# Performance work log

Measured on AMD Instinct MI355X. Metric: run time of the kernel, lower is better.

The kernel has to match this reference:

```python
import jax, jax.numpy as jnp
import numpy as np

N_NODES = 50000
N_EDGES = 800000
IN_DIM = 128
HID_DIM = 128
N_CLS = 64
EPS = 1e-12  # torch F.normalize clamp_min eps


def setup_inputs() -> dict:
    key = jax.random.key(0)
    ks = jax.random.split(key, 10)
    x = jax.random.normal(ks[0], (N_NODES, IN_DIM), dtype=jnp.float32)
    edge_index = jax.random.randint(ks[1], (2, N_EDGES), 0, N_NODES, dtype=jnp.int64)
    C_vals = jax.random.uniform(ks[2], (N_EDGES,), dtype=jnp.float32)
    W1 = jax.random.normal(ks[3], (IN_DIM, HID_DIM), dtype=jnp.float32) * 0.05
    b1 = jax.random.normal(ks[4], (HID_DIM,), dtype=jnp.float32) * 0.05
    W2 = jax.random.normal(ks[5], (HID_DIM, HID_DIM), dtype=jnp.float32) * 0.05
    b2 = jax.random.normal(ks[6], (HID_DIM,), dtype=jnp.float32) * 0.05
    W3 = jax.random.normal(ks[7], (HID_DIM, N_CLS), dtype=jnp.float32) * 0.05
    b3 = jax.random.normal(ks[8], (N_CLS,), dtype=jnp.float32) * 0.05
    return {"x": x, "edge_index": edge_index, "C_vals": C_vals,
            "W1": W1, "b1": b1, "W2": W2, "b2": b2, "W3": W3, "b3": b3}


def _spmm(row, col, vals, h, n):
    # C @ h with C sparse COO: out[row] += vals * h[col]
    return jax.ops.segment_sum(vals[:, None] * h[col], row, num_segments=n)


def reference(x, edge_index, C_vals, W1, b1, W2, b2, W3, b3):
    n = x.shape[0]
    row, col = edge_index[0], edge_index[1]

    def layer(h, W, b, last):
        prop = _spmm(row, col, C_vals, h, n)          # [N, d_in]
        h = prop @ W + b                              # Linear
        if not last:
            h = jax.nn.relu(h)
            # dropout inactive in eval mode; L2 normalize rows (norm=True)
            nrm = jnp.maximum(jnp.linalg.norm(h, axis=1, keepdims=True), EPS)
            h = h / nrm
        return h

    h = layer(x, W1, b1, False)
    h = layer(h, W2, b2, False)
    h = layer(h, W3, b3, True)
    return h
```

## Files before the change

kernel.cpp:

```cpp
#include <hip/hip_runtime.h>
#include <hip/hip_fp16.h>

#define NN 50000
#define NE 800000
#define DIM 128
#define NB ((NN + 255) / 256)

typedef _Float16 half8 __attribute__((ext_vector_type(8)));
typedef float f32x4 __attribute__((ext_vector_type(4)));

__global__ __launch_bounds__(256) void edge_histo_pos(const int* __restrict__ ei,
                                                      int* __restrict__ cnt,
                                                      int* __restrict__ pos) {
  int e = blockIdx.x * 256 + threadIdx.x;
  if (e >= NE) return;
  int r = ei[e], c = ei[NE + e];
  int p = -1;
  if ((unsigned)r < NN && (unsigned)c < NN) p = atomicAdd(&cnt[r], 1);
  pos[e] = p;
}

__global__ __launch_bounds__(256) void block_sums(const int* __restrict__ cnt,
                                                  int* __restrict__ bsum) {
  int i = blockIdx.x * 256 + threadIdx.x;
  int v = (i < NN) ? cnt[i] : 0;
#pragma unroll
  for (int off = 1; off < 64; off <<= 1) v += __shfl_xor(v, off, 64);
  __shared__ int ws[4];
  if ((threadIdx.x & 63) == 0) ws[threadIdx.x >> 6] = v;
  __syncthreads();
  if (threadIdx.x == 0) bsum[blockIdx.x] = ws[0] + ws[1] + ws[2] + ws[3];
}

__global__ __launch_bounds__(256) void scan_bsums(const int* __restrict__ bsum,
                                                  int* __restrict__ bbase) {
  int t = threadIdx.x;
  int v = (t < NB) ? bsum[t] : 0;
  int lane = t & 63, w = t >> 6;
  int inc = v;
#pragma unroll
  for (int off = 1; off < 64; off <<= 1) {
    int u = __shfl_up(inc, off, 64);
    if (lane >= off) inc += u;
  }
  __shared__ int ws[4];
  if (lane == 63) ws[w] = inc;
  __syncthreads();
  int wb = 0;
  for (int k = 0; k < w; ++k) wb += ws[k];
  if (t < NB) bbase[t] = wb + inc - v;
}

__global__ __launch_bounds__(256) void scan_final(const int* __restrict__ cnt,
                                                  const int* __restrict__ bbase,
                                                  int* __restrict__ rowStart) {
  int i = blockIdx.x * 256 + threadIdx.x;
  int v = (i < NN) ? cnt[i] : 0;
  int lane = threadIdx.x & 63, w = threadIdx.x >> 6;
  int inc = v;
#pragma unroll
  for (int off = 1; off < 64; off <<= 1) {
    int u = __shfl_up(inc, off, 64);
    if (lane >= off) inc += u;
  }
  __shared__ int ws[4];
  if (lane == 63) ws[w] = inc;
  __syncthreads();
  int wb = 0;
  for (int k = 0; k < w; ++k) wb += ws[k];
  int ex = bbase[blockIdx.x] + wb + inc - v;
  if (i < NN) rowStart[i] = ex;
  if (i == NN - 1) rowStart[NN] = ex + v;
}

__global__ __launch_bounds__(256) void edge_scatter(const int* __restrict__ ei,
                                                    const float* __restrict__ vals,
                                                    const int* __restrict__ rowStart,
                                                    const int* __restrict__ pos,
                                                    int2* __restrict__ cv) {
  int e = blockIdx.x * 256 + threadIdx.x;
  if (e >= NE) return;
  int p = pos[e];
  if (p < 0) return;
  int r = ei[e], c = ei[NE + e];
  cv[rowStart[r] + p] = make_int2(c, __float_as_int(vals[e]));
}

__global__ __launch_bounds__(256) void f32_to_f16(const float* __restrict__ src,
                                                  __half* __restrict__ dst, int n4) {
  int i = blockIdx.x * 256 + threadIdx.x;
  if (i >= n4) return;
  float4 v = ((const float4*)src)[i];
  __half2 lo = __floats2half2_rn(v.x, v.y);
  __half2 hi = __floats2half2_rn(v.z, v.w);
  uint2 u;
  u.x = *(unsigned int*)&lo;
  u.y = *(unsigned int*)&hi;
  ((uint2*)dst)[i] = u;
}

__global__ __launch_bounds__(256) void pack_w(const float* __restrict__ W,
                                              __half* __restrict__ Wp, int N, int total) {
  int idx = blockIdx.x * 256 + threadIdx.x;
  if (idx >= total) return;
  int j = idx & 7, lane = (idx >> 3) & 63, ctkt = idx >> 9;
  int NC = N / 16;
  int kt = ctkt / NC, ct = ctkt - kt * NC;
  int k = kt * 32 + ((lane >> 4) << 3) + j;
  int n = ct * 16 + (lane & 15);
  Wp[idx] = __float2half(W[k * N + n]);
}

__device__ __forceinline__ void fma4(float v, const float4& x, float4& acc) {
  acc.x = fmaf(v, x.x, acc.x);
  acc.y = fmaf(v, x.y, acc.y);
  acc.z = fmaf(v, x.z, acc.z);
  acc.w = fmaf(v, x.w, acc.w);
}

__device__ __forceinline__ float4 cvt4(uint2 raw) {
  __half2 a = *reinterpret_cast<__half2*>(&raw.x);
  __half2 b = *reinterpret_cast<__half2*>(&raw.y);
  float2 fa = __half22float2(a), fb = __half22float2(b);
  return make_float4(fa.x, fa.y, fb.x, fb.y);
}

template <int D, bool BIAS, bool HOUT>
__global__ __launch_bounds__(256) void spmm_csr_h(const int* __restrict__ rowStart,
                                                  const int2* __restrict__ cv,
                                                  const __half* __restrict__ h,
                                                  const float* __restrict__ bias,
                                                  void* __restrict__ outv) {
  constexpr int L = D / 4;
  const int lane = threadIdx.x % L;
  const int r = blockIdx.x * (256 / L) + threadIdx.x / L;
  if (r >= NN) return;
  int p = rowStart[r], pend = rowStart[r + 1];
  float4 acc = BIAS ? ((const float4*)bias)[lane] : make_float4(0.f, 0.f, 0.f, 0.f);
  for (; p + 7 < pend; p += 8) {
    int2 e0 = cv[p],     e1 = cv[p + 1], e2 = cv[p + 2], e3 = cv[p + 3];
    int2 e4 = cv[p + 4], e5 = cv[p + 5], e6 = cv[p + 6], e7 = cv[p + 7];
    uint2 r0 = ((const uint2*)(h + (size_t)e0.x * D))[lane];
    uint2 r1 = ((const uint2*)(h + (size_t)e1.x * D))[lane];
    uint2 r2 = ((const uint2*)(h + (size_t)e2.x * D))[lane];
    uint2 r3 = ((const uint2*)(h + (size_t)e3.x * D))[lane];
    uint2 r4 = ((const uint2*)(h + (size_t)e4.x * D))[lane];
    uint2 r5 = ((const uint2*)(h + (size_t)e5.x * D))[lane];
    uint2 r6 = ((const uint2*)(h + (size_t)e6.x * D))[lane];
    uint2 r7 = ((const uint2*)(h + (size_t)e7.x * D))[lane];
    fma4(__int_as_float(e0.y), cvt4(r0), acc);
    fma4(__int_as_float(e1.y), cvt4(r1), acc);
    fma4(__int_as_float(e2.y), cvt4(r2), acc);
    fma4(__int_as_float(e3.y), cvt4(r3), acc);
    fma4(__int_as_float(e4.y), cvt4(r4), acc);
    fma4(__int_as_float(e5.y), cvt4(r5), acc);
    fma4(__int_as_float(e6.y), cvt4(r6), acc);
    fma4(__int_as_float(e7.y), cvt4(r7), acc);
  }
  for (; p < pend; ++p) {
    int2 e0 = cv[p];
    uint2 r0 = ((const uint2*)(h + (size_t)e0.x * D))[lane];
    fma4(__int_as_float(e0.y), cvt4(r0), acc);
  }
  if (HOUT) {
    __half2 lo = __floats2half2_rn(acc.x, acc.y);
    __half2 hi = __floats2half2_rn(acc.z, acc.w);
    uint2 u;
    u.x = *(unsigned int*)&lo;
    u.y = *(unsigned int*)&hi;
    ((uint2*)((__half*)outv + (size_t)r * D))[lane] = u;
  } else {
    ((float4*)((float*)outv + (size_t)r * D))[lane] = acc;
  }
}

template <int NOUT, bool NORM, bool BIAS>
__global__ __launch_bounds__(256) void gemm_mfma(const __half* __restrict__ A,
                                                 const __half* __restrict__ Wp,
                                                 const float* __restrict__ b,
                                                 __half* __restrict__ out, int n) {
  constexpr int NC = NOUT / 16;
  constexpr int KT = DIM / 32;
  __shared__ __half Ws[KT * NC * 64 * 8];
  const int tid = threadIdx.x;
  for (int i = tid; i < KT * NC * 64; i += 256)
    ((half8*)Ws)[i] = ((const half8*)Wp)[i];
  __syncthreads();

  const int wid = tid >> 6, lane = tid & 63;
  const int colbase = lane & 15;
  const int kgrp = lane >> 4;
  const int ntiles = (n + 63) >> 6;

  for (int tile = blockIdx.x; tile < ntiles; tile += gridDim.x) {
    const int row0 = tile * 64 + wid * 16;
    int rowA = row0 + colbase;
    if (rowA > n - 1) rowA = n - 1;
    const half8* Arow = (const half8*)(A + (size_t)rowA * DIM);

    f32x4 acc[NC];
#pragma unroll
    for (int ct = 0; ct < NC; ++ct) {
      float bv = BIAS ? b[ct * 16 + colbase] : 0.f;
      acc[ct] = (f32x4){bv, bv, bv, bv};
    }

#pragma unroll
    for (int kt = 0; kt < KT; ++kt) {
      half8 af = Arow[kt * 4 + kgrp];
#pragma unroll
      for (int ct = 0; ct < NC; ++ct) {
        half8 bf = ((const half8*)Ws)[(kt * NC + ct) * 64 + lane];
        acc[ct] = __builtin_amdgcn_mfma_f32_16x16x32_f16(af, bf, acc[ct], 0, 0, 0);
      }
    }

#pragma unroll
    for (int j = 0; j < 4; ++j) {
      int row = row0 + (kgrp << 2) + j;
      if (NORM) {
        float s = 0.f;
#pragma unroll
        for (int ct = 0; ct < NC; ++ct) {
          float v = fmaxf(acc[ct][j], 0.f);
          s = fmaf(v, v, s);
        }
        s += __shfl_xor(s, 1); s += __shfl_xor(s, 2);
        s += __shfl_xor(s, 4); s += __shfl_xor(s, 8);
        float inv = 1.0f / fmaxf(sqrtf(s), 1e-12f);
        if (row < n) {
#pragma unroll
          for (int ct = 0; ct < NC; ++ct)
            out[(size_t)row * NOUT + ct * 16 + colbase] =
                __float2half(fmaxf(acc[ct][j], 0.f) * inv);
        }
      } else {
        if (row < n) {
#pragma unroll
          for (int ct = 0; ct < NC; ++ct)
            out[(size_t)row * NOUT + ct * 16 + colbase] = __float2half(acc[ct][j]);
        }
      }
    }
  }
}

__global__ __launch_bounds__(256) void spmm_atomic(
    const int* __restrict__ ei, const float* __restrict__ vals,
    const float* __restrict__ h, float* __restrict__ prop) {
  const int lane32 = threadIdx.x & 31;
  int hw = blockIdx.x * (blockDim.x >> 5) + (threadIdx.x >> 5);
  const int stride = gridDim.x * (blockDim.x >> 5);
  for (int e = hw; e < NE; e += stride) {
    int r = ei[e], c = ei[NE + e];
    float v = vals[e];
    if ((unsigned)r >= NN || (unsigned)c >= NN) continue;
    float4 x = ((const float4*)(h + (size_t)c * DIM))[lane32];
    float* pp = prop + (size_t)r * DIM + lane32 * 4;
    unsafeAtomicAdd(pp + 0, v * x.x);
    unsafeAtomicAdd(pp + 1, v * x.y);
    unsafeAtomicAdd(pp + 2, v * x.z);
    unsafeAtomicAdd(pp + 3, v * x.w);
  }
}

template <int OUT_DIM, int MR, bool NORM, bool BIAS>
__global__ __launch_bounds__(256) void gemm_lds2(
    const float* __restrict__ A, const float* __restrict__ W,
    const float* __restrict__ b, float* __restrict__ out, int n) {
  constexpr int JT = OUT_DIM / 4;
  constexpr int RG = 256 / JT;
  constexpr int TILE_M = RG * MR;
  __shared__ float Ws[DIM * OUT_DIM];
  __shared__ float As[TILE_M * DIM];
  const int tid = threadIdx.x;
  for (int i = tid; i < DIM * OUT_DIM / 4; i += 256)
    ((float4*)Ws)[i] = ((const float4*)W)[i];
  const int j = tid % JT, rg = tid / JT;
  float4 bv = make_float4(0.f, 0.f, 0.f, 0.f);
  if (BIAS) bv = ((const float4*)b)[j];
  const float* Wj = Ws + j * 4;
  const int ntiles = (n + TILE_M - 1) / TILE_M;
  for (int tile = blockIdx.x; tile < ntiles; tile += gridDim.x) {
    const size_t gbase = (size_t)tile * TILE_M * DIM;
#pragma unroll
    for (int it = 0; it < 4; ++it) {
      const float* g = A + gbase + it * 1024 + tid * 4;
      auto* lp = (__attribute__((address_space(3))) char*)As + it * 4096 + (tid >> 6) * 1024;
      __builtin_amdgcn_global_load_lds((const __attribute__((address_space(1))) void*)g,
                                       (__attribute__((address_space(3))) void*)lp, 16, 0, 0);
    }
    asm volatile("s_waitcnt vmcnt(0)" ::: "memory");
    __syncthreads();
    float acc[MR][4];
#pragma unroll
    for (int i = 0; i < MR; ++i) {
      acc[i][0] = bv.x; acc[i][1] = bv.y; acc[i][2] = bv.z; acc[i][3] = bv.w;
    }
#pragma unroll 2
    for (int kk = 0; kk < DIM; kk += 4) {
      float4 w0 = *(const float4*)(Wj + (size_t)(kk + 0) * OUT_DIM);
      float4 w1 = *(const float4*)(Wj + (size_t)(kk + 1) * OUT_DIM);
      float4 w2 = *(const float4*)(Wj + (size_t)(kk + 2) * OUT_DIM);
      float4 w3 = *(const float4*)(Wj + (size_t)(kk + 3) * OUT_DIM);
      float4 a4[MR];
#pragma unroll
      for (int i = 0; i < MR; ++i)
        a4[i] = *(const float4*)(As + (rg * MR + i) * DIM + kk);
#pragma unroll
      for (int i = 0; i < MR; ++i) {
        acc[i][0] = fmaf(a4[i].x, w0.x, acc[i][0]);
        acc[i][1] = fmaf(a4[i].x, w0.y, acc[i][1]);
        acc[i][2] = fmaf(a4[i].x, w0.z, acc[i][2]);
        acc[i][3] = fmaf(a4[i].x, w0.w, acc[i][3]);
        acc[i][0] = fmaf(a4[i].y, w1.x, acc[i][0]);
        acc[i][1] = fmaf(a4[i].y, w1.y, acc[i][1]);
        acc[i][2] = fmaf(a4[i].y, w1.z, acc[i][2]);
        acc[i][3] = fmaf(a4[i].y, w1.w, acc[i][3]);
        acc[i][0] = fmaf(a4[i].z, w2.x, acc[i][0]);
        acc[i][1] = fmaf(a4[i].z, w2.y, acc[i][1]);
        acc[i][2] = fmaf(a4[i].z, w2.z, acc[i][2]);
        acc[i][3] = fmaf(a4[i].z, w2.w, acc[i][3]);
        acc[i][0] = fmaf(a4[i].w, w3.x, acc[i][0]);
        acc[i][1] = fmaf(a4[i].w, w3.y, acc[i][1]);
        acc[i][2] = fmaf(a4[i].w, w3.z, acc[i][2]);
        acc[i][3] = fmaf(a4[i].w, w3.w, acc[i][3]);
      }
    }
    const int row0 = tile * TILE_M + rg * MR;
#pragma unroll
    for (int i = 0; i < MR; ++i) {
      int row = row0 + i;
      float v0 = acc[i][0], v1 = acc[i][1], v2 = acc[i][2], v3 = acc[i][3];
      if (NORM) {
        v0 = fmaxf(v0, 0.f); v1 = fmaxf(v1, 0.f);
        v2 = fmaxf(v2, 0.f); v3 = fmaxf(v3, 0.f);
        float s = v0 * v0 + v1 * v1 + v2 * v2 + v3 * v3;
#pragma unroll
        for (int off = JT / 2; off >= 1; off >>= 1) s += __shfl_xor(s, off, JT);
        float inv = 1.0f / fmaxf(sqrtf(s), 1e-12f);
        v0 *= inv; v1 *= inv; v2 *= inv; v3 *= inv;
      }
      if (row < n)
        ((float4*)(out + (size_t)row * OUT_DIM))[j] = make_float4(v0, v1, v2, v3);
    }
    __syncthreads();
  }
}

extern "C" void kernel_launch(void* const* d_in, const int* in_sizes, int n_in,
                              void* d_out, int out_size, void* d_ws, size_t ws_size,
                              hipStream_t stream) {
  const float* x  = (const float*)d_in[0];
  const int*   ei = (const int*)d_in[1];
  const float* C  = (const float*)d_in[2];
  const float* W1 = (const float*)d_in[3];
  const float* b1 = (const float*)d_in[4];
  const float* W2 = (const float*)d_in[5];
  const float* b2 = (const float*)d_in[6];
  const float* W3 = (const float*)d_in[7];
  const float* b3 = (const float*)d_in[8];
  float* out = (float*)d_out;

  __half* prop16   = (__half*)d_ws;
  __half* h16      = prop16 + (size_t)NN * DIM;
  __half* x16      = h16 + (size_t)NN * DIM;
  __half* Wp1      = x16 + (size_t)NN * DIM;
  __half* Wp2      = Wp1 + 16384;
  __half* Wp3      = Wp2 + 16384;
  int*    rowStart = (int*)(Wp3 + 8192);
  int*    cnt      = rowStart + NN + 2;
  int*    bsum     = cnt + NN;
  int*    bbase    = bsum + 256;
  int*    pos      = bbase + 256;
  int2*   cv       = (int2*)(pos + NE);
  const size_t need = (size_t)(3 * NN * DIM) * 2 + 40960 * 2 +
                      (size_t)(2 * NN + 2 + 512) * 4 + (size_t)NE * 4 + (size_t)NE * 8;

  const dim3 blk(256);
  const int gEdge = (NE + 255) / 256;
  const int gTiles = (NN + 63) / 64;

  if (ws_size >= need) {
    f32_to_f16<<<(NN * DIM / 4 + 255) / 256, blk, 0, stream>>>(x, x16, NN * DIM / 4);
    pack_w<<<(16384 + 255) / 256, blk, 0, stream>>>(W1, Wp1, 128, 16384);
    pack_w<<<(16384 + 255) / 256, blk, 0, stream>>>(W2, Wp2, 128, 16384);
    pack_w<<<(8192 + 255) / 256, blk, 0, stream>>>(W3, Wp3, 64, 8192);

    hipMemsetAsync(cnt, 0, (size_t)NN * 4, stream);
    edge_histo_pos<<<gEdge, blk, 0, stream>>>(ei, cnt, pos);
    block_sums<<<NB, blk, 0, stream>>>(cnt, bsum);
    scan_bsums<<<1, blk, 0, stream>>>(bsum, bbase);
    scan_final<<<NB, blk, 0, stream>>>(cnt, bbase, rowStart);
    edge_scatter<<<gEdge, blk, 0, stream>>>(ei, C, rowStart, pos, cv);

    spmm_csr_h<128, false, true><<<(NN + 7) / 8, blk, 0, stream>>>(rowStart, cv, x16, nullptr, prop16);
    gemm_mfma<128, true, true><<<gTiles, blk, 0, stream>>>(prop16, Wp1, b1, h16, NN);
    spmm_csr_h<128, false, true><<<(NN + 7) / 8, blk, 0, stream>>>(rowStart, cv, h16, nullptr, prop16);
    __half* hh16 = x16;
    gemm_mfma<128, true, true><<<gTiles, blk, 0, stream>>>(prop16, Wp2, b2, hh16, NN);
    __half* g16 = h16;
    gemm_mfma<64, false, false><<<gTiles, blk, 0, stream>>>(hh16, Wp3, nullptr, g16, NN);
    spmm_csr_h<64, true, false><<<(NN + 15) / 16, blk, 0, stream>>>(rowStart, cv, g16, b3, out);
  } else {
    float* prop = (float*)d_ws;
    float* h    = prop + (size_t)NN * DIM;
    const size_t propBytes = (size_t)NN * DIM * sizeof(float);
    const int spmmGrid = 4096;
    hipMemsetAsync(prop, 0, propBytes, stream);
    spmm_atomic<<<spmmGrid, blk, 0, stream>>>(ei, C, x, prop);
    gemm_lds2<128, 4, true, true><<<512, blk, 0, stream>>>(prop, W1, b1, h, NN);
    hipMemsetAsync(prop, 0, propBytes, stream);
    spmm_atomic<<<spmmGrid, blk, 0, stream>>>(ei, C, h, prop);
    gemm_lds2<128, 4, true, true><<<512, blk, 0, stream>>>(prop, W2, b2, h, NN);
    hipMemsetAsync(prop, 0, propBytes, stream);
    spmm_atomic<<<spmmGrid, blk, 0, stream>>>(ei, C, h, prop);
    gemm_lds2<64, 2, false, true><<<768, blk, 0, stream>>>(prop, W3, b3, out, NN);
  }
}
```

Baseline: 197.3 us.

## Fuse CSR SpMM with MFMA GEMM per tile and merge prep/scan kernels

Layers 1 and 2 now run SpMM and the MFMA GEMM with ReLU and L2-normalize in one persistent kernel. Each 64-row tile of propagated features is staged in padded LDS instead of being written to and read back from a global fp16 buffer. The x conversion and three weight-packing launches become one prep kernel, and the two-level scan drops a single-block kernel by having each block sum the preceding block totals itself. The trade-off is lower parallelism during the gather, since only 768 blocks run and each half-wave handles 8 rows serially with a smaller unroll. The fallback path is also simplified.

```diff
diff --git a/kernel.cpp b/kernel.cpp
--- a/kernel.cpp
+++ b/kernel.cpp
@@ -5,6 +5,8 @@
 #define NE 800000
 #define DIM 128
 #define NB ((NN + 255) / 256)
+#define N4 (NN * DIM / 4)
+#define APAD 8
 
 typedef _Float16 half8 __attribute__((ext_vector_type(8)));
 typedef float f32x4 __attribute__((ext_vector_type(4)));
@@ -32,10 +34,20 @@
   if (threadIdx.x == 0) bsum[blockIdx.x] = ws[0] + ws[1] + ws[2] + ws[3];
 }
 
-__global__ __launch_bounds__(256) void scan_bsums(const int* __restrict__ bsum,
-                                                  int* __restrict__ bbase) {
-  int t = threadIdx.x;
-  int v = (t < NB) ? bsum[t] : 0;
+__global__ __launch_bounds__(256) void scan_final2(const int* __restrict__ cnt,
+                                                   const int* __restrict__ bsum,
+                                                   int* __restrict__ rowStart) {
+  const int t = threadIdx.x, bid = blockIdx.x;
+  int s = (t < bid && t < NB) ? bsum[t] : 0;
+#pragma unroll
+  for (int off = 1; off < 64; off <<= 1) s += __shfl_xor(s, off, 64);
+  __shared__ int wsum[4];
+  if ((t & 63) == 0) wsum[t >> 6] = s;
+  __syncthreads();
+  const int base = wsum[0] + wsum[1] + wsum[2] + wsum[3];
+
+  int i = bid * 256 + t;
+  int v = (i < NN) ? cnt[i] : 0;
   int lane = t & 63, w = t >> 6;
   int inc = v;
 #pragma unroll
@@ -48,27 +60,7 @@
   __syncthreads();
   int wb = 0;
   for (int k = 0; k < w; ++k) wb += ws[k];
-  if (t < NB) bbase[t] = wb + inc - v;
-}
-
-__global__ __launch_bounds__(256) void scan_final(const int* __restrict__ cnt,
-                                                  const int* __restrict__ bbase,
-                                                  int* __restrict__ rowStart) {
-  int i = blockIdx.x * 256 + threadIdx.x;
-  int v = (i < NN) ? cnt[i] : 0;
-  int lane = threadIdx.x & 63, w = threadIdx.x >> 6;
-  int inc = v;
-#pragma unroll
-  for (int off = 1; off < 64; off <<= 1) {
-    int u = __shfl_up(inc, off, 64);
-    if (lane >= off) inc += u;
-  }
-  __shared__ int ws[4];
-  if (lane == 63) ws[w] = inc;
-  __syncthreads();
-  int wb = 0;
-  for (int k = 0; k < w; ++k) wb += ws[k];
-  int ex = bbase[blockIdx.x] + wb + inc - v;
+  int ex = base + wb + inc - v;
   if (i < NN) rowStart[i] = ex;
   if (i == NN - 1) rowStart[NN] = ex + v;
 }
@@ -86,23 +78,8 @@
   cv[rowStart[r] + p] = make_int2(c, __float_as_int(vals[e]));
 }
 
-__global__ __launch_bounds__(256) void f32_to_f16(const float* __restrict__ src,
-                                                  __half* __restrict__ dst, int n4) {
-  int i = blockIdx.x * 256 + threadIdx.x;
-  if (i >= n4) return;
-  float4 v = ((const float4*)src)[i];
-  __half2 lo = __floats2half2_rn(v.x, v.y);
-  __half2 hi = __floats2half2_rn(v.z, v.w);
-  uint2 u;
-  u.x = *(unsigned int*)&lo;
-  u.y = *(unsigned int*)&hi;
-  ((uint2*)dst)[i] = u;
-}
-
-__global__ __launch_bounds__(256) void pack_w(const float* __restrict__ W,
-                                              __half* __restrict__ Wp, int N, int total) {
-  int idx = blockIdx.x * 256 + threadIdx.x;
-  if (idx >= total) return;
+__device__ __forceinline__ void pack_one(const float* __restrict__ W,
+                                         __half* __restrict__ Wp, int N, int idx) {
   int j = idx & 7, lane = (idx >> 3) & 63, ctkt = idx >> 9;
   int NC = N / 16;
   int kt = ctkt / NC, ct = ctkt - kt * NC;
@@ -111,6 +88,33 @@
   Wp[idx] = __float2half(W[k * N + n]);
 }
 
+__global__ __launch_bounds__(256) void prep(const float* __restrict__ x,
+                                            const float* __restrict__ W1,
+                                            const float* __restrict__ W2,
+                                            const float* __restrict__ W3,
+                                            __half* __restrict__ x16,
+                                            __half* __restrict__ Wp1,
+                                            __half* __restrict__ Wp2,
+                                            __half* __restrict__ Wp3) {
+  int idx = blockIdx.x * 256 + threadIdx.x;
+  if (idx < N4) {
+    float4 v = ((const float4*)x)[idx];
+    __half2 lo = __floats2half2_rn(v.x, v.y);
+    __half2 hi = __floats2half2_rn(v.z, v.w);
+    uint2 u;
+    u.x = *(unsigned int*)&lo;
+    u.y = *(unsigned int*)&hi;
+    ((uint2*)x16)[idx] = u;
+    return;
+  }
+  int k = idx - N4;
+  if (k < 16384) { pack_one(W1, Wp1, 128, k); return; }
+  k -= 16384;
+  if (k < 16384) { pack_one(W2, Wp2, 128, k); return; }
+  k -= 16384;
+  if (k < 8192) pack_one(W3, Wp3, 64, k);
+}
+
 __device__ __forceinline__ void fma4(float v, const float4& x, float4& acc) {
   acc.x = fmaf(v, x.x, acc.x);
   acc.y = fmaf(v, x.y, acc.y);
@@ -125,59 +129,102 @@
   return make_float4(fa.x, fa.y, fb.x, fb.y);
 }
 
-template <int D, bool BIAS, bool HOUT>
-__global__ __launch_bounds__(256) void spmm_csr_h(const int* __restrict__ rowStart,
-                                                  const int2* __restrict__ cv,
-                                                  const __half* __restrict__ h,
-                                                  const float* __restrict__ bias,
-                                                  void* __restrict__ outv) {
-  constexpr int L = D / 4;
-  const int lane = threadIdx.x % L;
-  const int r = blockIdx.x * (256 / L) + threadIdx.x / L;
-  if (r >= NN) return;
-  int p = rowStart[r], pend = rowStart[r + 1];
-  float4 acc = BIAS ? ((const float4*)bias)[lane] : make_float4(0.f, 0.f, 0.f, 0.f);
-  for (; p + 7 < pend; p += 8) {
-    int2 e0 = cv[p],     e1 = cv[p + 1], e2 = cv[p + 2], e3 = cv[p + 3];
-    int2 e4 = cv[p + 4], e5 = cv[p + 5], e6 = cv[p + 6], e7 = cv[p + 7];
-    uint2 r0 = ((const uint2*)(h + (size_t)e0.x * D))[lane];
-    uint2 r1 = ((const uint2*)(h + (size_t)e1.x * D))[lane];
-    uint2 r2 = ((const uint2*)(h + (size_t)e2.x * D))[lane];
-    uint2 r3 = ((const uint2*)(h + (size_t)e3.x * D))[lane];
-    uint2 r4 = ((const uint2*)(h + (size_t)e4.x * D))[lane];
-    uint2 r5 = ((const uint2*)(h + (size_t)e5.x * D))[lane];
-    uint2 r6 = ((const uint2*)(h + (size_t)e6.x * D))[lane];
-    uint2 r7 = ((const uint2*)(h + (size_t)e7.x * D))[lane];
-    fma4(__int_as_float(e0.y), cvt4(r0), acc);
-    fma4(__int_as_float(e1.y), cvt4(r1), acc);
-    fma4(__int_as_float(e2.y), cvt4(r2), acc);
-    fma4(__int_as_float(e3.y), cvt4(r3), acc);
-    fma4(__int_as_float(e4.y), cvt4(r4), acc);
-    fma4(__int_as_float(e5.y), cvt4(r5), acc);
-    fma4(__int_as_float(e6.y), cvt4(r6), acc);
-    fma4(__int_as_float(e7.y), cvt4(r7), acc);
-  }
-  for (; p < pend; ++p) {
-    int2 e0 = cv[p];
-    uint2 r0 = ((const uint2*)(h + (size_t)e0.x * D))[lane];
-    fma4(__int_as_float(e0.y), cvt4(r0), acc);
-  }
-  if (HOUT) {
-    __half2 lo = __floats2half2_rn(acc.x, acc.y);
-    __half2 hi = __floats2half2_rn(acc.z, acc.w);
-    uint2 u;
-    u.x = *(unsigned int*)&lo;
-    u.y = *(unsigned int*)&hi;
-    ((uint2*)((__half*)outv + (size_t)r * D))[lane] = u;
-  } else {
-    ((float4*)((float*)outv + (size_t)r * D))[lane] = acc;
-  }
-}
-
-template <int NOUT, bool NORM, bool BIAS>
+template <bool FIRST>
+__global__ __launch_bounds__(256) void fused_spmm_gemm(const int* __restrict__ rowStart,
+                                                       const int2* __restrict__ cv,
+                                                       const __half* __restrict__ h,
+                                                       const __half* __restrict__ Wp,
+                                                       const float* __restrict__ b,
+                                                       __half* __restrict__ out, int n) {
+  constexpr int NC = DIM / 16;
+  constexpr int KT = DIM / 32;
+  __shared__ __half Ws[KT * NC * 64 * 8];
+  __shared__ __half As[64 * (DIM + APAD)];
+  const int tid = threadIdx.x;
+  for (int i = tid; i < KT * NC * 64; i += 256)
+    ((half8*)Ws)[i] = ((const half8*)Wp)[i];
+
+  const int hw = tid >> 5, lane32 = tid & 31;
+  const int wid = tid >> 6, lane = tid & 63;
+  const int colbase = lane & 15, kgrp = lane >> 4;
+  const int ntiles = (n + 63) >> 6;
+
+  for (int tile = blockIdx.x; tile < ntiles; tile += gridDim.x) {
+#pragma unroll
+    for (int rr = 0; rr < 8; ++rr) {
+      const int lrow = hw * 8 + rr;
+      const int row = tile * 64 + lrow;
+      float4 acc = make_float4(0.f, 0.f, 0.f, 0.f);
+      if (row < n) {
+        int p = rowStart[row], pend = rowStart[row + 1];
+        for (; p + 3 < pend; p += 4) {
+          int2 e0 = cv[p], e1 = cv[p + 1], e2 = cv[p + 2], e3 = cv[p + 3];
+          uint2 r0 = ((const uint2*)(h + (size_t)e0.x * DIM))[lane32];
+          uint2 r1 = ((const uint2*)(h + (size_t)e1.x * DIM))[lane32];
+          uint2 r2 = ((const uint2*)(h + (size_t)e2.x * DIM))[lane32];
+          uint2 r3 = ((const uint2*)(h + (size_t)e3.x * DIM))[lane32];
+          fma4(__int_as_float(e0.y), cvt4(r0), acc);
+          fma4(__int_as_float(e1.y), cvt4(r1), acc);
+          fma4(__int_as_float(e2.y), cvt4(r2), acc);
+          fma4(__int_as_float(e3.y), cvt4(r3), acc);
+        }
+        for (; p < pend; ++p) {
+          int2 e0 = cv[p];
+          uint2 r0 = ((const uint2*)(h + (size_t)e0.x * DIM))[lane32];
+          fma4(__int_as_float(e0.y), cvt4(r0), acc);
+        }
+      }
+      __half2 lo = __floats2half2_rn(acc.x, acc.y);
+      __half2 hi = __floats2half2_rn(acc.z, acc.w);
+      uint2 u;
+      u.x = *(unsigned int*)&lo;
+      u.y = *(unsigned int*)&hi;
+      *(uint2*)(As + lrow * (DIM + APAD) + lane32 * 4) = u;
+    }
+    __syncthreads();
+
+    f32x4 acc2[NC];
+#pragma unroll
+    for (int ct = 0; ct < NC; ++ct) {
+      float bv = b[ct * 16 + colbase];
+      acc2[ct] = (f32x4){bv, bv, bv, bv};
+    }
+#pragma unroll
+    for (int kt = 0; kt < KT; ++kt) {
+      half8 af = *(const half8*)(As + (wid * 16 + colbase) * (DIM + APAD) + kt * 32 + kgrp * 8);
+#pragma unroll
+      for (int ct = 0; ct < NC; ++ct) {
+        half8 bf = ((const half8*)Ws)[(kt * NC + ct) * 64 + lane];
+        acc2[ct] = __builtin_amdgcn_mfma_f32_16x16x32_f16(af, bf, acc2[ct], 0, 0, 0);
+      }
+    }
+    const int row0 = tile * 64 + wid * 16;
+#pragma unroll
+    for (int j = 0; j < 4; ++j) {
+      int row = row0 + (kgrp << 2) + j;
+      float s = 0.f;
+#pragma unroll
+      for (int ct = 0; ct < NC; ++ct) {
+        float v = fmaxf(acc2[ct][j], 0.f);
+        s = fmaf(v, v, s);
+      }
+      s += __shfl_xor(s, 1); s += __shfl_xor(s, 2);
+      s += __shfl_xor(s, 4); s += __shfl_xor(s, 8);
+      float inv = 1.0f / fmaxf(sqrtf(s), 1e-12f);
+      if (row < n) {
+#pragma unroll
+        for (int ct = 0; ct < NC; ++ct)
+          out[(size_t)row * DIM + ct * 16 + colbase] =
+              __float2half(fmaxf(acc2[ct][j], 0.f) * inv);
+      }
+    }
+    __syncthreads();
+  }
+}
+
+template <int NOUT>
 __global__ __launch_bounds__(256) void gemm_mfma(const __half* __restrict__ A,
                                                  const __half* __restrict__ Wp,
-                                                 const float* __restrict__ b,
                                                  __half* __restrict__ out, int n) {
   constexpr int NC = NOUT / 16;
   constexpr int KT = DIM / 32;
@@ -188,8 +235,7 @@
   __syncthreads();
 
   const int wid = tid >> 6, lane = tid & 63;
-  const int colbase = lane & 15;
-  const int kgrp = lane >> 4;
+  const int colbase = lane & 15, kgrp = lane >> 4;
   const int ntiles = (n + 63) >> 6;
 
   for (int tile = blockIdx.x; tile < ntiles; tile += gridDim.x) {
@@ -197,14 +243,9 @@
     int rowA = row0 + colbase;
     if (rowA > n - 1) rowA = n - 1;
     const half8* Arow = (const half8*)(A + (size_t)rowA * DIM);
-
     f32x4 acc[NC];
 #pragma unroll
-    for (int ct = 0; ct < NC; ++ct) {
-      float bv = BIAS ? b[ct * 16 + colbase] : 0.f;
-      acc[ct] = (f32x4){bv, bv, bv, bv};
-    }
-
+    for (int ct = 0; ct < NC; ++ct) acc[ct] = (f32x4){0.f, 0.f, 0.f, 0.f};
 #pragma unroll
     for (int kt = 0; kt < KT; ++kt) {
       half8 af = Arow[kt * 4 + kgrp];
@@ -214,35 +255,47 @@
         acc[ct] = __builtin_amdgcn_mfma_f32_16x16x32_f16(af, bf, acc[ct], 0, 0, 0);
       }
     }
-
 #pragma unroll
     for (int j = 0; j < 4; ++j) {
       int row = row0 + (kgrp << 2) + j;
-      if (NORM) {
-        float s = 0.f;
-#pragma unroll
-        for (int ct = 0; ct < NC; ++ct) {
-          float v = fmaxf(acc[ct][j], 0.f);
-          s = fmaf(v, v, s);
-        }
-        s += __shfl_xor(s, 1); s += __shfl_xor(s, 2);
-        s += __shfl_xor(s, 4); s += __shfl_xor(s, 8);
-        float inv = 1.0f / fmaxf(sqrtf(s), 1e-12f);
-        if (row < n) {
-#pragma unroll
-          for (int ct = 0; ct < NC; ++ct)
-            out[(size_t)row * NOUT + ct * 16 + colbase] =
-                __float2half(fmaxf(acc[ct][j], 0.f) * inv);
-        }
-      } else {
-        if (row < n) {
-#pragma unroll
-          for (int ct = 0; ct < NC; ++ct)
-            out[(size_t)row * NOUT + ct * 16 + colbase] = __float2half(acc[ct][j]);
-        }
-      }
-    }
-  }
+      if (row < n) {
+#pragma unroll
+        for (int ct = 0; ct < NC; ++ct)
+          out[(size_t)row * NOUT + ct * 16 + colbase] = __float2half(acc[ct][j]);
+      }
+    }
+  }
+}
+
+template <int D>
+__global__ __launch_bounds__(256) void spmm_csr_f(const int* __restrict__ rowStart,
+                                                  const int2* __restrict__ cv,
+                                                  const __half* __restrict__ h,
+                                                  const float* __restrict__ bias,
+                                                  float* __restrict__ out) {
+  constexpr int L = D / 4;
+  const int lane = threadIdx.x % L;
+  const int r = blockIdx.x * (256 / L) + threadIdx.x / L;
+  if (r >= NN) return;
+  int p = rowStart[r], pend = rowStart[r + 1];
+  float4 acc = ((const float4*)bias)[lane];
+  for (; p + 3 < pend; p += 4) {
+    int2 e0 = cv[p], e1 = cv[p + 1], e2 = cv[p + 2], e3 = cv[p + 3];
+    uint2 r0 = ((const uint2*)(h + (size_t)e0.x * D))[lane];
+    uint2 r1 = ((const uint2*)(h + (size_t)e1.x * D))[lane];
+    uint2 r2 = ((const uint2*)(h + (size_t)e2.x * D))[lane];
+    uint2 r3 = ((const uint2*)(h + (size_t)e3.x * D))[lane];
+    fma4(__int_as_float(e0.y), cvt4(r0), acc);
+    fma4(__int_as_float(e1.y), cvt4(r1), acc);
+    fma4(__int_as_float(e2.y), cvt4(r2), acc);
+    fma4(__int_as_float(e3.y), cvt4(r3), acc);
+  }
+  for (; p < pend; ++p) {
+    int2 e0 = cv[p];
+    uint2 r0 = ((const uint2*)(h + (size_t)e0.x * D))[lane];
+    fma4(__int_as_float(e0.y), cvt4(r0), acc);
+  }
+  ((float4*)(out + (size_t)r * D))[lane] = acc;
 }
 
 __global__ __launch_bounds__(256) void spmm_atomic(
@@ -264,87 +317,54 @@
   }
 }
 
-template <int OUT_DIM, int MR, bool NORM, bool BIAS>
-__global__ __launch_bounds__(256) void gemm_lds2(
+template <int OUT_DIM, int MR, bool NORM>
+__global__ __launch_bounds__(256) void gemm_fb(
     const float* __restrict__ A, const float* __restrict__ W,
     const float* __restrict__ b, float* __restrict__ out, int n) {
   constexpr int JT = OUT_DIM / 4;
   constexpr int RG = 256 / JT;
   constexpr int TILE_M = RG * MR;
-  __shared__ float Ws[DIM * OUT_DIM];
-  __shared__ float As[TILE_M * DIM];
-  const int tid = threadIdx.x;
-  for (int i = tid; i < DIM * OUT_DIM / 4; i += 256)
-    ((float4*)Ws)[i] = ((const float4*)W)[i];
-  const int j = tid % JT, rg = tid / JT;
-  float4 bv = make_float4(0.f, 0.f, 0.f, 0.f);
-  if (BIAS) bv = ((const float4*)b)[j];
-  const float* Wj = Ws + j * 4;
-  const int ntiles = (n + TILE_M - 1) / TILE_M;
-  for (int tile = blockIdx.x; tile < ntiles; tile += gridDim.x) {
-    const size_t gbase = (size_t)tile * TILE_M * DIM;
-#pragma unroll
-    for (int it = 0; it < 4; ++it) {
-      const float* g = A + gbase + it * 1024 + tid * 4;
-      auto* lp = (__attribute__((address_space(3))) char*)As + it * 4096 + (tid >> 6) * 1024;
-      __builtin_amdgcn_global_load_lds((const __attribute__((address_space(1))) void*)g,
-                                       (__attribute__((address_space(3))) void*)lp, 16, 0, 0);
-    }
-    asm volatile("s_waitcnt vmcnt(0)" ::: "memory");
-    __syncthreads();
-    float acc[MR][4];
+  const int j = threadIdx.x % JT, rg = threadIdx.x / JT;
+  const int row0 = blockIdx.x * TILE_M + rg * MR;
+  float4 bv = ((const float4*)b)[j];
+  float acc[MR][4];
+#pragma unroll
+  for (int i = 0; i < MR; ++i) {
+    acc[i][0] = bv.x; acc[i][1] = bv.y; acc[i][2] = bv.z; acc[i][3] = bv.w;
+  }
+  const float* Arow[MR];
+#pragma unroll
+  for (int i = 0; i < MR; ++i) {
+    int r = row0 + i; if (r > n - 1) r = n - 1;
+    Arow[i] = A + (size_t)r * DIM;
+  }
+  for (int kk = 0; kk < DIM; ++kk) {
+    const float* Wr = W + (size_t)kk * OUT_DIM + j * 4;
+    float4 w = *(const float4*)Wr;
 #pragma unroll
     for (int i = 0; i < MR; ++i) {
-      acc[i][0] = bv.x; acc[i][1] = bv.y; acc[i][2] = bv.z; acc[i][3] = bv.w;
-    }
-#pragma unroll 2
-    for (int kk = 0; kk < DIM; kk += 4) {
-      float4 w0 = *(const float4*)(Wj + (size_t)(kk + 0) * OUT_DIM);
-      float4 w1 = *(const float4*)(Wj + (size_t)(kk + 1) * OUT_DIM);
-      float4 w2 = *(const float4*)(Wj + (size_t)(kk + 2) * OUT_DIM);
-      float4 w3 = *(const float4*)(Wj + (size_t)(kk + 3) * OUT_DIM);
-      float4 a4[MR];
-#pragma unroll
-      for (int i = 0; i < MR; ++i)
-        a4[i] = *(const float4*)(As + (rg * MR + i) * DIM + kk);
-#pragma unroll
-      for (int i = 0; i < MR; ++i) {
-        acc[i][0] = fmaf(a4[i].x, w0.x, acc[i][0]);
-        acc[i][1] = fmaf(a4[i].x, w0.y, acc[i][1]);
-        acc[i][2] = fmaf(a4[i].x, w0.z, acc[i][2]);
-        acc[i][3] = fmaf(a4[i].x, w0.w, acc[i][3]);
-        acc[i][0] = fmaf(a4[i].y, w1.x, acc[i][0]);
-        acc[i][1] = fmaf(a4[i].y, w1.y, acc[i][1]);
-        acc[i][2] = fmaf(a4[i].y, w1.z, acc[i][2]);
-        acc[i][3] = fmaf(a4[i].y, w1.w, acc[i][3]);
-        acc[i][0] = fmaf(a4[i].z, w2.x, acc[i][0]);
-        acc[i][1] = fmaf(a4[i].z, w2.y, acc[i][1]);
-        acc[i][2] = fmaf(a4[i].z, w2.z, acc[i][2]);
-        acc[i][3] = fmaf(a4[i].z, w2.w, acc[i][3]);
-        acc[i][0] = fmaf(a4[i].w, w3.x, acc[i][0]);
-        acc[i][1] = fmaf(a4[i].w, w3.y, acc[i][1]);
-        acc[i][2] = fmaf(a4[i].w, w3.z, acc[i][2]);
-        acc[i][3] = fmaf(a4[i].w, w3.w, acc[i][3]);
-      }
-    }
-    const int row0 = tile * TILE_M + rg * MR;
-#pragma unroll
-    for (int i = 0; i < MR; ++i) {
-      int row = row0 + i;
-      float v0 = acc[i][0], v1 = acc[i][1], v2 = acc[i][2], v3 = acc[i][3];
-      if (NORM) {
-        v0 = fmaxf(v0, 0.f); v1 = fmaxf(v1, 0.f);
-        v2 = fmaxf(v2, 0.f); v3 = fmaxf(v3, 0.f);
-        float s = v0 * v0 + v1 * v1 + v2 * v2 + v3 * v3;
-#pragma unroll
-        for (int off = JT / 2; off >= 1; off >>= 1) s += __shfl_xor(s, off, JT);
-        float inv = 1.0f / fmaxf(sqrtf(s), 1e-12f);
-        v0 *= inv; v1 *= inv; v2 *= inv; v3 *= inv;
-      }
-      if (row < n)
-        ((float4*)(out + (size_t)row * OUT_DIM))[j] = make_float4(v0, v1, v2, v3);
-    }
-    __syncthreads();
+      float a = Arow[i][kk];
+      acc[i][0] = fmaf(a, w.x, acc[i][0]);
+      acc[i][1] = fmaf(a, w.y, acc[i][1]);
+      acc[i][2] = fmaf(a, w.z, acc[i][2]);
+      acc[i][3] = fmaf(a, w.w, acc[i][3]);
+    }
+  }
+#pragma unroll
+  for (int i = 0; i < MR; ++i) {
+    int row = row0 + i;
+    float v0 = acc[i][0], v1 = acc[i][1], v2 = acc[i][2], v3 = acc[i][3];
+    if (NORM) {
+      v0 = fmaxf(v0, 0.f); v1 = fmaxf(v1, 0.f);
+      v2 = fmaxf(v2, 0.f); v3 = fmaxf(v3, 0.f);
+      float s = v0 * v0 + v1 * v1 + v2 * v2 + v3 * v3;
+#pragma unroll
+      for (int off = JT / 2; off >= 1; off >>= 1) s += __shfl_xor(s, off, JT);
+      float inv = 1.0f / fmaxf(sqrtf(s), 1e-12f);
+      v0 *= inv; v1 *= inv; v2 *= inv; v3 *= inv;
+    }
+    if (row < n)
+      ((float4*)(out + (size_t)row * OUT_DIM))[j] = make_float4(v0, v1, v2, v3);
   }
 }
 
@@ -362,59 +382,50 @@
   const float* b3 = (const float*)d_in[8];
   float* out = (float*)d_out;
 
-  __half* prop16   = (__half*)d_ws;
-  __half* h16      = prop16 + (size_t)NN * DIM;
-  __half* x16      = h16 + (size_t)NN * DIM;
-  __half* Wp1      = x16 + (size_t)NN * DIM;
+  __half* x16      = (__half*)d_ws;
+  __half* h16      = x16 + (size_t)NN * DIM;
+  __half* Wp1      = h16 + (size_t)NN * DIM;
   __half* Wp2      = Wp1 + 16384;
   __half* Wp3      = Wp2 + 16384;
   int*    rowStart = (int*)(Wp3 + 8192);
   int*    cnt      = rowStart + NN + 2;
   int*    bsum     = cnt + NN;
-  int*    bbase    = bsum + 256;
-  int*    pos      = bbase + 256;
+  int*    pos      = bsum + 256;
   int2*   cv       = (int2*)(pos + NE);
-  const size_t need = (size_t)(3 * NN * DIM) * 2 + 40960 * 2 +
-                      (size_t)(2 * NN + 2 + 512) * 4 + (size_t)NE * 4 + (size_t)NE * 8;
+  const size_t need = (size_t)(2 * NN * DIM) * 2 + 40960 * 2 +
+                      (size_t)(2 * NN + 2 + 256) * 4 + (size_t)NE * 4 + (size_t)NE * 8;
 
   const dim3 blk(256);
   const int gEdge = (NE + 255) / 256;
+  const int gFused = 768;
   const int gTiles = (NN + 63) / 64;
 
   if (ws_size >= need) {
-    f32_to_f16<<<(NN * DIM / 4 + 255) / 256, blk, 0, stream>>>(x, x16, NN * DIM / 4);
-    pack_w<<<(16384 + 255) / 256, blk, 0, stream>>>(W1, Wp1, 128, 16384);
-    pack_w<<<(16384 + 255) / 256, blk, 0, stream>>>(W2, Wp2, 128, 16384);
-    pack_w<<<(8192 + 255) / 256, blk, 0, stream>>>(W3, Wp3, 64, 8192);
-
+    prep<<<(N4 + 40960 + 255) / 256, blk, 0, stream>>>(x, W1, W2, W3, x16, Wp1, Wp2, Wp3);
     hipMemsetAsync(cnt, 0, (size_t)NN * 4, stream);
     edge_histo_pos<<<gEdge, blk, 0, stream>>>(ei, cnt, pos);
     block_sums<<<NB, blk, 0, stream>>>(cnt, bsum);
-    scan_bsums<<<1, blk, 0, stream>>>(bsum, bbase);
-    scan_final<<<NB, blk, 0, stream>>>(cnt, bbase, rowStart);
+    scan_final2<<<NB, blk, 0, stream>>>(cnt, bsum, rowStart);
     edge_scatter<<<gEdge, blk, 0, stream>>>(ei, C, rowStart, pos, cv);
 
-    spmm_csr_h<128, false, true><<<(NN + 7) / 8, blk, 0, stream>>>(rowStart, cv, x16, nullptr, prop16);
-    gemm_mfma<128, true, true><<<gTiles, blk, 0, stream>>>(prop16, Wp1, b1, h16, NN);
-    spmm_csr_h<128, false, true><<<(NN + 7) / 8, blk, 0, stream>>>(rowStart, cv, h16, nullptr, prop16);
+    fused_spmm_gemm<true><<<gFused, blk, 0, stream>>>(rowStart, cv, x16, Wp1, b1, h16, NN);
     __half* hh16 = x16;
-    gemm_mfma<128, true, true><<<gTiles, blk, 0, stream>>>(prop16, Wp2, b2, hh16, NN);
+    fused_spmm_gemm<false><<<gFused, blk, 0, stream>>>(rowStart, cv, h16, Wp2, b2, hh16, NN);
     __half* g16 = h16;
-    gemm_mfma<64, false, false><<<gTiles, blk, 0, stream>>>(hh16, Wp3, nullptr, g16, NN);
-    spmm_csr_h<64, true, false><<<(NN + 15) / 16, blk, 0, stream>>>(rowStart, cv, g16, b3, out);
+    gemm_mfma<64><<<gTiles, blk, 0, stream>>>(hh16, Wp3, g16, NN);
+    spmm_csr_f<64><<<(NN + 15) / 16, blk, 0, stream>>>(rowStart, cv, g16, b3, out);
   } else {
     float* prop = (float*)d_ws;
     float* h    = prop + (size_t)NN * DIM;
     const size_t propBytes = (size_t)NN * DIM * sizeof(float);
-    const int spmmGrid = 4096;
     hipMemsetAsync(prop, 0, propBytes, stream);
-    spmm_atomic<<<spmmGrid, blk, 0, stream>>>(ei, C, x, prop);
-    gemm_lds2<128, 4, true, true><<<512, blk, 0, stream>>>(prop, W1, b1, h, NN);
+    spmm_atomic<<<4096, blk, 0, stream>>>(ei, C, x, prop);
+    gemm_fb<128, 4, true><<<(NN + 31) / 32, blk, 0, stream>>>(prop, W1, b1, h, NN);
     hipMemsetAsync(prop, 0, propBytes, stream);
-    spmm_atomic<<<spmmGrid, blk, 0, stream>>>(ei, C, h, prop);
-    gemm_lds2<128, 4, true, true><<<512, blk, 0, stream>>>(prop, W2, b2, h, NN);
+    spmm_atomic<<<4096, blk, 0, stream>>>(ei, C, h, prop);
+    gemm_fb<128, 4, true><<<(NN + 31) / 32, blk, 0, stream>>>(prop, W2, b2, h, NN);
     hipMemsetAsync(prop, 0, propBytes, stream);
-    spmm_atomic<<<spmmGrid, blk, 0, stream>>>(ei, C, h, prop);
-    gemm_lds2<64, 2, false, true><<<768, blk, 0, stream>>>(prop, W3, b3, out, NN);
-  }
-}
+    spmm_atomic<<<4096, blk, 0, stream>>>(ei, C, h, prop);
+    gemm_fb<64, 2, false><<<(NN + 31) / 32, blk, 0, stream>>>(prop, W3, b3, out, NN);
+  }
+}
```

After: 271.2 us. 37.5% more time.
